# Kernel tuning notes

Hardware: AMD Instinct MI355X
Metric: run time of the kernel (lower is better)

The kernel has to match this reference:

```python
import jax, jax.numpy as jnp
import numpy as np

D_MODEL = 512
SEQ_LEN = 2048
S = 32  # local window size
BATCH = 2


def setup_inputs() -> dict:
    key = jax.random.key(0)
    ks = jax.random.split(key, 12)
    shp = (SEQ_LEN, BATCH, D_MODEL)
    return {
        "query": jax.random.normal(ks[0], shp, jnp.float32),
        "key": jax.random.normal(ks[1], shp, jnp.float32),
        "value": jax.random.normal(ks[2], shp, jnp.float32),
        "Wq": jax.random.normal(ks[3], (D_MODEL, D_MODEL), jnp.float32) * 0.02,
        "bq": jax.random.normal(ks[4], (D_MODEL,), jnp.float32) * 0.01,
        "Wk": jax.random.normal(ks[5], (D_MODEL, D_MODEL), jnp.float32) * 0.02,
        "bk": jax.random.normal(ks[6], (D_MODEL,), jnp.float32) * 0.01,
        "Wv": jax.random.normal(ks[7], (D_MODEL, D_MODEL), jnp.float32) * 0.02,
        "bv": jax.random.normal(ks[8], (D_MODEL,), jnp.float32) * 0.01,
        "pos_bias": jax.random.normal(ks[9], (SEQ_LEN, SEQ_LEN), jnp.float32) * 0.02,
        "Wo": jax.random.normal(ks[10], (D_MODEL, D_MODEL), jnp.float32) * 0.02,
        "bo": jax.random.normal(ks[11], (D_MODEL,), jnp.float32) * 0.01,
    }


def _aft_local(query, key, value, Wq, bq, Wk, bk, Wv, bv, pos_bias, Wo, bo):
    T, B, D = query.shape
    q = query @ Wq.T + bq  # [T,B,D]
    k = key @ Wk.T + bk
    v = value @ Wv.T + bv
    pb = pos_bias[:T, :T]

    # max_logit: elementwise max of per-dim key max and (key + col-max of pos_bias) max,
    # then batch index 0 (faithful to original `[0]` indexing) -> shape [D]
    max_logit = jnp.maximum(k.max(axis=0),
                            (k + pb.max(axis=0)[:, None, None]).max(axis=0))[0]

    # out-of-window running sums: tokens t' <= t - S contribute exp(k) (no pos bias)
    ek = jnp.exp(k - max_logit)                 # [T,B,D]
    cs_num = jnp.cumsum(ek * v, axis=0)
    cs_den = jnp.cumsum(ek, axis=0)
    t_arr = jnp.arange(T)
    prefix_idx = jnp.clip(t_arr - S, 0, T - 1)
    has_prefix = (t_arr >= S)[:, None, None]
    num_out = jnp.where(has_prefix, cs_num[prefix_idx], 0.0)
    den_out = jnp.where(has_prefix, cs_den[prefix_idx], 0.0)

    # in-window part: t' in [max(0, t-S+1), t] with pos_bias[t, t']
    j = jnp.arange(S)
    idx_raw = t_arr[:, None] - S + 1 + j[None, :]   # [T,S]
    valid = (idx_raw >= 0).astype(k.dtype)
    idx = jnp.clip(idx_raw, 0, T - 1)
    k_win = k[idx]                                  # [T,S,B,D]
    v_win = v[idx]                                  # [T,S,B,D]
    pb_win = pb[t_arr[:, None], idx]                # [T,S]
    exp_l = jnp.exp(k_win + pb_win[:, :, None, None] - max_logit) * valid[:, :, None, None]
    num_in = (exp_l * v_win).sum(axis=1)            # [T,B,D]
    den_in = exp_l.sum(axis=1)

    y = jax.nn.sigmoid(q) * (num_out + num_in) / (den_out + den_in)
    return y @ Wo.T + bo


def reference(query, key, value, Wq, bq, Wk, bk, Wv, bv, pos_bias, Wo, bo):
    return _aft_local(query, key, value, Wq, bq, Wk, bk, Wv, bv, pos_bias, Wo, bo)
```

## Files before the change

kernel.cpp:

```cpp
#include <hip/hip_runtime.h>
#include <hip/hip_bf16.h>

#define TT 2048
#define BB 2
#define DD 512
#define BD (BB*DD)
#define SS 32
#define MR (TT*BB)
#define NE (TT*BB*DD)
#define CH 32

typedef __bf16 bf16x8 __attribute__((ext_vector_type(8)));
typedef float f32x4 __attribute__((ext_vector_type(4)));
typedef float f32x2 __attribute__((ext_vector_type(2)));

__device__ __forceinline__ void async_copy16(void* lds, const void* gptr) {
    __builtin_amdgcn_global_load_lds(
        (const __attribute__((address_space(1))) void*)gptr,
        (__attribute__((address_space(3))) void*)lds,
        16, 0, 0);
}

#define MFMA16(a,b,c) __builtin_amdgcn_mfma_f32_16x16x32_bf16((a),(b),(c),0,0,0)

__global__ __launch_bounds__(256) void cast_all(
    const float* __restrict__ s0, const float* __restrict__ s1, const float* __restrict__ s2,
    const float* __restrict__ w0, const float* __restrict__ w1,
    const float* __restrict__ w2, const float* __restrict__ w3,
    __hip_bfloat16* __restrict__ d0, __hip_bfloat16* __restrict__ d1, __hip_bfloat16* __restrict__ d2,
    __hip_bfloat16* __restrict__ e0, __hip_bfloat16* __restrict__ e1,
    __hip_bfloat16* __restrict__ e2, __hip_bfloat16* __restrict__ e3)
{
    int b = blockIdx.x;
    const float* s;
    __hip_bfloat16* d;
    size_t i;
    if (b < 6144) {
        int which = b >> 11;
        s = which == 0 ? s0 : (which == 1 ? s1 : s2);
        d = which == 0 ? d0 : (which == 1 ? d1 : d2);
        i = ((size_t)(b & 2047) * 256 + threadIdx.x) * 4;
    } else {
        int b2 = b - 6144;
        int which = b2 >> 8;
        s = which == 0 ? w0 : (which == 1 ? w1 : (which == 2 ? w2 : w3));
        d = which == 0 ? e0 : (which == 1 ? e1 : (which == 2 ? e2 : e3));
        i = ((size_t)(b2 & 255) * 256 + threadIdx.x) * 4;
    }
    float4 f = *(const float4*)(s + i);
    union { __hip_bfloat16 h[4]; ushort4 u; } cv;
    cv.h[0] = __float2bfloat16(f.x); cv.h[1] = __float2bfloat16(f.y);
    cv.h[2] = __float2bfloat16(f.z); cv.h[3] = __float2bfloat16(f.w);
    *(ushort4*)((unsigned short*)d + i) = cv.u;
}

__global__ __launch_bounds__(256) void gemm_qkv(
    const __hip_bfloat16* __restrict__ qb, const __hip_bfloat16* __restrict__ kb,
    const __hip_bfloat16* __restrict__ vb,
    const __hip_bfloat16* __restrict__ Wqb, const __hip_bfloat16* __restrict__ Wkb,
    const __hip_bfloat16* __restrict__ Wvb,
    const float* __restrict__ bq, const float* __restrict__ bk,
    const float* __restrict__ bv,
    float* __restrict__ qout, float* __restrict__ ekn,
    float* __restrict__ part)
{
    __shared__ char smem[49152];
    const int tid = threadIdx.x;
    const int lane = tid & 63;
    const int wv = tid >> 6;
    const int wave_m = wv >> 1, wave_n = wv & 1;
    const int m0 = blockIdx.y * 64, n0 = blockIdx.x * 64;
    const int kq = lane >> 4, rr = lane & 15;

    if (blockIdx.z == 0) {
        f32x4 acc[2][2] = {};
        const __hip_bfloat16* Arow = qb + (size_t)(m0 + lane) * DD + wv * 8;
        const __hip_bfloat16* Wrow = Wqb + (size_t)(n0 + lane) * DD + wv * 8;
        async_copy16(smem + 0*8192 +        wv*1024, Arow + 0);
        async_copy16(smem + 0*8192 + 4096 + wv*1024, Wrow + 0);
        async_copy16(smem + 1*8192 +        wv*1024, Arow + 32);
        async_copy16(smem + 1*8192 + 4096 + wv*1024, Wrow + 32);
        asm volatile("s_waitcnt vmcnt(2)" ::: "memory");
        __builtin_amdgcn_s_barrier();
        #pragma unroll
        for (int it = 0; it < 16; ++it) {
            if (it + 2 < 16) {
                char* nb = smem + ((it + 2) % 3) * 8192;
                async_copy16(nb +        wv*1024, Arow + (it+2)*32);
                async_copy16(nb + 4096 + wv*1024, Wrow + (it+2)*32);
            }
            const char* cb = smem + (it % 3) * 8192;
            bf16x8 a0 = *(const bf16x8*)(cb + kq*1024 + (wave_m*32 +  0 + rr)*16);
            bf16x8 a1 = *(const bf16x8*)(cb + kq*1024 + (wave_m*32 + 16 + rr)*16);
            bf16x8 w0 = *(const bf16x8*)(cb + 4096 + kq*1024 + (wave_n*32 +  0 + rr)*16);
            bf16x8 w1 = *(const bf16x8*)(cb + 4096 + kq*1024 + (wave_n*32 + 16 + rr)*16);
            acc[0][0] = MFMA16(a0, w0, acc[0][0]);
            acc[0][1] = MFMA16(a0, w1, acc[0][1]);
            acc[1][0] = MFMA16(a1, w0, acc[1][0]);
            acc[1][1] = MFMA16(a1, w1, acc[1][1]);
            if (it < 15) {
                if (it < 14) asm volatile("s_waitcnt vmcnt(2) lgkmcnt(0)" ::: "memory");
                else         asm volatile("s_waitcnt vmcnt(0) lgkmcnt(0)" ::: "memory");
                __builtin_amdgcn_s_barrier();
            }
        }
        #pragma unroll
        for (int ms = 0; ms < 2; ++ms)
            #pragma unroll
            for (int ns = 0; ns < 2; ++ns) {
                int n = n0 + wave_n*32 + ns*16 + rr;
                float bn = bq[n];
                #pragma unroll
                for (int r = 0; r < 4; ++r) {
                    int m = m0 + wave_m*32 + ms*16 + kq*4 + r;
                    qout[(size_t)m * DD + n] = acc[ms][ns][r] + bn;
                }
            }
    } else {
        f32x4 acck[2][2] = {}, accv[2][2] = {};
        const __hip_bfloat16* AKrow = kb + (size_t)(m0 + lane) * DD + wv * 8;
        const __hip_bfloat16* WKrow = Wkb + (size_t)(n0 + lane) * DD + wv * 8;
        const __hip_bfloat16* AVrow = vb + (size_t)(m0 + lane) * DD + wv * 8;
        const __hip_bfloat16* WVrow = Wvb + (size_t)(n0 + lane) * DD + wv * 8;
        #pragma unroll
        for (int pt = 0; pt < 2; ++pt) {
            char* nb = smem + pt * 16384;
            async_copy16(nb +         wv*1024, AKrow + pt*32);
            async_copy16(nb +  4096 + wv*1024, WKrow + pt*32);
            async_copy16(nb +  8192 + wv*1024, AVrow + pt*32);
            async_copy16(nb + 12288 + wv*1024, WVrow + pt*32);
        }
        asm volatile("s_waitcnt vmcnt(4)" ::: "memory");
        __builtin_amdgcn_s_barrier();
        #pragma unroll
        for (int it = 0; it < 16; ++it) {
            if (it + 2 < 16) {
                char* nb = smem + ((it + 2) % 3) * 16384;
                async_copy16(nb +         wv*1024, AKrow + (it+2)*32);
                async_copy16(nb +  4096 + wv*1024, WKrow + (it+2)*32);
                async_copy16(nb +  8192 + wv*1024, AVrow + (it+2)*32);
                async_copy16(nb + 12288 + wv*1024, WVrow + (it+2)*32);
            }
            const char* cb = smem + (it % 3) * 16384;
            bf16x8 ak0 = *(const bf16x8*)(cb +         kq*1024 + (wave_m*32 +  0 + rr)*16);
            bf16x8 ak1 = *(const bf16x8*)(cb +         kq*1024 + (wave_m*32 + 16 + rr)*16);
            bf16x8 bk0 = *(const bf16x8*)(cb +  4096 + kq*1024 + (wave_n*32 +  0 + rr)*16);
            bf16x8 bk1 = *(const bf16x8*)(cb +  4096 + kq*1024 + (wave_n*32 + 16 + rr)*16);
            bf16x8 av0 = *(const bf16x8*)(cb +  8192 + kq*1024 + (wave_m*32 +  0 + rr)*16);
            bf16x8 av1 = *(const bf16x8*)(cb +  8192 + kq*1024 + (wave_m*32 + 16 + rr)*16);
            bf16x8 bv0 = *(const bf16x8*)(cb + 12288 + kq*1024 + (wave_n*32 +  0 + rr)*16);
            bf16x8 bv1 = *(const bf16x8*)(cb + 12288 + kq*1024 + (wave_n*32 + 16 + rr)*16);
            acck[0][0] = MFMA16(ak0, bk0, acck[0][0]);
            acck[0][1] = MFMA16(ak0, bk1, acck[0][1]);
            acck[1][0] = MFMA16(ak1, bk0, acck[1][0]);
            acck[1][1] = MFMA16(ak1, bk1, acck[1][1]);
            accv[0][0] = MFMA16(av0, bv0, accv[0][0]);
            accv[0][1] = MFMA16(av0, bv1, accv[0][1]);
            accv[1][0] = MFMA16(av1, bv0, accv[1][0]);
            accv[1][1] = MFMA16(av1, bv1, accv[1][1]);
            if (it < 15) {
                if (it < 14) asm volatile("s_waitcnt vmcnt(4) lgkmcnt(0)" ::: "memory");
                else         asm volatile("s_waitcnt vmcnt(0) lgkmcnt(0)" ::: "memory");
                __builtin_amdgcn_s_barrier();
            }
        }
        float sd[2][2] = {{0.f,0.f},{0.f,0.f}};
        float sn[2][2] = {{0.f,0.f},{0.f,0.f}};
        #pragma unroll
        for (int ms = 0; ms < 2; ++ms)
            #pragma unroll
            for (int ns = 0; ns < 2; ++ns) {
                int n = n0 + wave_n*32 + ns*16 + rr;
                float bkn = bk[n], bvn = bv[n];
                #pragma unroll
                for (int r = 0; r < 4; ++r) {
                    int m = m0 + wave_m*32 + ms*16 + kq*4 + r;
                    float e  = expf(acck[ms][ns][r] + bkn);
                    float nv = e * (accv[ms][ns][r] + bvn);
                    float2 st; st.x = e; st.y = nv;
                    *(float2*)&ekn[((size_t)m * DD + n) * 2] = st;
                    sd[ns][r & 1] += e;
                    sn[ns][r & 1] += nv;
                }
            }
        #pragma unroll
        for (int ns = 0; ns < 2; ++ns)
            #pragma unroll
            for (int par = 0; par < 2; ++par) {
                sd[ns][par] += __shfl_xor(sd[ns][par], 16, 64);
                sd[ns][par] += __shfl_xor(sd[ns][par], 32, 64);
                sn[ns][par] += __shfl_xor(sn[ns][par], 16, 64);
                sn[ns][par] += __shfl_xor(sn[ns][par], 32, 64);
            }
        __syncthreads();
        float* red = (float*)smem;
        if (lane < 16) {
            #pragma unroll
            for (int ns = 0; ns < 2; ++ns) {
                int c2 = wave_n*32 + ns*16 + rr;
                red[(0*2 + wave_m)*64 + c2] = sd[ns][0];
                red[(1*2 + wave_m)*64 + c2] = sd[ns][1];
                red[(2*2 + wave_m)*64 + c2] = sn[ns][0];
                red[(3*2 + wave_m)*64 + c2] = sn[ns][1];
            }
        }
        __syncthreads();
        {
            int which = tid >> 6;
            int c2 = tid & 63;
            float s = red[(which*2 + 0)*64 + c2] + red[(which*2 + 1)*64 + c2];
            int b = which & 1;
            int sel = which >> 1;
            part[((size_t)blockIdx.y * BD + b*512 + n0 + c2) * 2 + sel] = s;
        }
    }
}

__global__ __launch_bounds__(256, 1) void scan_part(
    const float* __restrict__ part, float* __restrict__ pref)
{
    const int col = blockIdx.x * 256 + threadIdx.x;
    f32x2 run = {0.f, 0.f};
    #pragma unroll
    for (int p0 = 0; p0 < 64; p0 += 8) {
        f32x2 v[8];
        #pragma unroll
        for (int u = 0; u < 8; ++u)
            v[u] = *(const f32x2*)&part[((size_t)(p0 + u) * BD + col) * 2];
        #pragma unroll
        for (int u = 0; u < 8; ++u) {
            *(f32x2*)&pref[((size_t)(p0 + u) * BD + col) * 2] = run;
            run += v[u];
        }
    }
}

__global__ __launch_bounds__(256, 3) void fused_window(
    const float* __restrict__ q, const float* __restrict__ ekn,
    const float* __restrict__ pref, const float* __restrict__ pb,
    __hip_bfloat16* __restrict__ yb)
{
    __shared__ float Et[64 * 64 * 2];
    __shared__ float wl[CH][SS];
    const int tid = threadIdx.x;
    const int chunk = blockIdx.y;
    const int t0 = chunk * CH;
    const int col0 = blockIdx.x * 64;
    const int c = tid & 63;
    const int sg = tid >> 6;
    const int s0 = sg * 8;

    {
        const int ub = tid >> 5;
        const int cp = tid & 31;
        #pragma unroll
        for (int j = 0; j < 8; ++j) {
            int u = ub + j * 8;
            int t = t0 - 32 + u;
            if (t >= 0) {
                const void* g = (const void*)(ekn + ((size_t)t * BD + col0 + cp * 2) * 2);
                async_copy16((char*)Et + (tid >> 6) * 1024 + j * 4096, g);
            }
        }
        if (chunk == 0) {
            f32x4 z = {0.f, 0.f, 0.f, 0.f};
            #pragma unroll
            for (int j = 0; j < 4; ++j)
                *(f32x4*)((char*)Et + tid * 16 + j * 4096) = z;
        }
    }

    #pragma unroll
    for (int i = 0; i < (CH * SS) / 256; ++i) {
        int idx = tid + i * 256;
        int tl = idx >> 5, jj = idx & 31;
        int t = t0 + tl;
        int u2 = t - (SS - 1) + jj;
        float w = 0.f;
        if (u2 >= 0) w = expf(pb[(size_t)t * TT + u2]);
        wl[tl][jj] = w;
    }

    float qv[8];
    #pragma unroll
    for (int k = 0; k < 8; ++k)
        qv[k] = q[(size_t)(t0 + s0 + k) * BD + col0 + c];
    f32x2 P = *(const f32x2*)&pref[((size_t)chunk * BD + col0 + c) * 2];

    __syncthreads();

    f32x2 ring[39];
    #pragma unroll
    for (int i = 0; i < 39; ++i)
        ring[i] = *(const f32x2*)&Et[((s0 + 1 + i) * 64 + c) * 2];

    f32x2 cs = P;
    #pragma unroll
    for (int u = 0; u < 31; ++u)
        if (u >= s0) cs -= ring[u - s0];

    #pragma unroll
    for (int k = 0; k < 8; ++k) {
        int s = s0 + k;
        if (k > 0) cs += ring[k - 1];
        f32x2 acc = cs;
        #pragma unroll
        for (int j4 = 0; j4 < 8; ++j4) {
            float4 w4 = *(const float4*)&wl[s][j4 * 4];
            acc += w4.x * ring[k + j4*4 + 0];
            acc += w4.y * ring[k + j4*4 + 1];
            acc += w4.z * ring[k + j4*4 + 2];
            acc += w4.w * ring[k + j4*4 + 3];
        }
        float sig = 1.f / (1.f + expf(-qv[k]));
        yb[(size_t)(t0 + s) * BD + col0 + c] = __float2bfloat16(sig * acc.y / acc.x);
    }
}

__global__ __launch_bounds__(256) void gemm_out(
    const __hip_bfloat16* __restrict__ yb, const __hip_bfloat16* __restrict__ Wob,
    const float* __restrict__ bo, float* __restrict__ out)
{
    __shared__ char smem[24576];
    const int tid = threadIdx.x;
    const int lane = tid & 63;
    const int wv = tid >> 6;
    const int wave_m = wv >> 1, wave_n = wv & 1;
    const int m0 = blockIdx.y * 64, n0 = blockIdx.x * 64;
    const int kq = lane >> 4, rr = lane & 15;

    f32x4 acc[2][2] = {};
    const __hip_bfloat16* Arow = yb + (size_t)(m0 + lane) * DD + wv * 8;
    const __hip_bfloat16* Wrow = Wob + (size_t)(n0 + lane) * DD + wv * 8;

    async_copy16(smem + 0*8192 +        wv*1024, Arow + 0);
    async_copy16(smem + 0*8192 + 4096 + wv*1024, Wrow + 0);
    async_copy16(smem + 1*8192 +        wv*1024, Arow + 32);
    async_copy16(smem + 1*8192 + 4096 + wv*1024, Wrow + 32);
    asm volatile("s_waitcnt vmcnt(2)" ::: "memory");
    __builtin_amdgcn_s_barrier();
    #pragma unroll
    for (int it = 0; it < 16; ++it) {
        if (it + 2 < 16) {
            char* nb = smem + ((it + 2) % 3) * 8192;
            async_copy16(nb +        wv*1024, Arow + (it+2)*32);
            async_copy16(nb + 4096 + wv*1024, Wrow + (it+2)*32);
        }
        const char* cb = smem + (it % 3) * 8192;
        bf16x8 a0 = *(const bf16x8*)(cb + kq*1024 + (wave_m*32 +  0 + rr)*16);
        bf16x8 a1 = *(const bf16x8*)(cb + kq*1024 + (wave_m*32 + 16 + rr)*16);
        bf16x8 w0 = *(const bf16x8*)(cb + 4096 + kq*1024 + (wave_n*32 +  0 + rr)*16);
        bf16x8 w1 = *(const bf16x8*)(cb + 4096 + kq*1024 + (wave_n*32 + 16 + rr)*16);
        acc[0][0] = MFMA16(a0, w0, acc[0][0]);
        acc[0][1] = MFMA16(a0, w1, acc[0][1]);
        acc[1][0] = MFMA16(a1, w0, acc[1][0]);
        acc[1][1] = MFMA16(a1, w1, acc[1][1]);
        if (it < 15) {
            if (it < 14) asm volatile("s_waitcnt vmcnt(2) lgkmcnt(0)" ::: "memory");
            else         asm volatile("s_waitcnt vmcnt(0) lgkmcnt(0)" ::: "memory");
            __builtin_amdgcn_s_barrier();
        }
    }
    #pragma unroll
    for (int ms = 0; ms < 2; ++ms)
        #pragma unroll
        for (int ns = 0; ns < 2; ++ns) {
            int n = n0 + wave_n*32 + ns*16 + rr;
            float bn = bo[n];
            #pragma unroll
            for (int r = 0; r < 4; ++r) {
                int m = m0 + wave_m*32 + ms*16 + kq*4 + r;
                out[(size_t)m * DD + n] = acc[ms][ns][r] + bn;
            }
        }
}

extern "C" void kernel_launch(void* const* d_in, const int* in_sizes, int n_in,
                              void* d_out, int out_size, void* d_ws, size_t ws_size,
                              hipStream_t stream) {
    const float* query = (const float*)d_in[0];
    const float* key   = (const float*)d_in[1];
    const float* value = (const float*)d_in[2];
    const float* Wq    = (const float*)d_in[3];
    const float* bq    = (const float*)d_in[4];
    const float* Wk    = (const float*)d_in[5];
    const float* bk    = (const float*)d_in[6];
    const float* Wv    = (const float*)d_in[7];
    const float* bv    = (const float*)d_in[8];
    const float* pb    = (const float*)d_in[9];
    const float* Wo    = (const float*)d_in[10];
    const float* bo    = (const float*)d_in[11];
    float* out = (float*)d_out;

    float* ws = (float*)d_ws;
    float* q    = ws;
    float* ekn  = ws + (size_t)NE;
    float* part = ws + (size_t)3 * NE;
    float* pref = part + 131072;
    __hip_bfloat16* bfb = (__hip_bfloat16*)(pref + 131072);
    __hip_bfloat16* qb  = bfb;
    __hip_bfloat16* kb  = bfb + (size_t)NE;
    __hip_bfloat16* vb  = bfb + (size_t)2 * NE;
    __hip_bfloat16* yb  = bfb + (size_t)3 * NE;
    __hip_bfloat16* Wqb = bfb + (size_t)4 * NE;
    __hip_bfloat16* Wkb = Wqb + 262144;
    __hip_bfloat16* Wvb = Wkb + 262144;
    __hip_bfloat16* Wob = Wvb + 262144;

    cast_all<<<7168, 256, 0, stream>>>(query, key, value, Wq, Wk, Wv, Wo,
                                       qb, kb, vb, Wqb, Wkb, Wvb, Wob);

    gemm_qkv<<<dim3(DD / 64, MR / 64, 2), 256, 0, stream>>>(
        qb, kb, vb, Wqb, Wkb, Wvb, bq, bk, bv,
        q, ekn, part);

    scan_part<<<4, 256, 0, stream>>>(part, pref);

    fused_window<<<dim3(BD / 64, TT / CH), 256, 0, stream>>>(
        q, ekn, pref, pb, yb);

    gemm_out<<<dim3(DD / 64, MR / 64), 256, 0, stream>>>(yb, Wob, bo, out);
}
```

Baseline: 190.3 us.

## Fuse all stages into one persistent kernel with atomic grid barriers

Replaces the five separate launches (cast, QKV GEMM, prefix scan, window kernel, output GEMM) with one persistent kernel of 512 blocks that moves between phases through atomic-counter grid barriers. The separate scan kernel is dropped: each window tile now sums the earlier per-chunk partials itself through a small LDS reduction. Each block runs both the K/V and Q GEMM tiles for its output tile in turn, and handles two window tiles. The aim is to cut launch and inter-kernel gaps, at the cost of serialising work inside each block. It also depends on all 512 blocks being co-resident (2 per CU), otherwise the spin barriers deadlock.

```diff
diff --git a/kernel.cpp b/kernel.cpp
--- a/kernel.cpp
+++ b/kernel.cpp
@@ -23,59 +23,333 @@
 
 #define MFMA16(a,b,c) __builtin_amdgcn_mfma_f32_16x16x32_bf16((a),(b),(c),0,0,0)
 
-__global__ __launch_bounds__(256) void cast_all(
-    const float* __restrict__ s0, const float* __restrict__ s1, const float* __restrict__ s2,
-    const float* __restrict__ w0, const float* __restrict__ w1,
-    const float* __restrict__ w2, const float* __restrict__ w3,
-    __hip_bfloat16* __restrict__ d0, __hip_bfloat16* __restrict__ d1, __hip_bfloat16* __restrict__ d2,
-    __hip_bfloat16* __restrict__ e0, __hip_bfloat16* __restrict__ e1,
-    __hip_bfloat16* __restrict__ e2, __hip_bfloat16* __restrict__ e3)
-{
-    int b = blockIdx.x;
-    const float* s;
-    __hip_bfloat16* d;
-    size_t i;
-    if (b < 6144) {
-        int which = b >> 11;
-        s = which == 0 ? s0 : (which == 1 ? s1 : s2);
-        d = which == 0 ? d0 : (which == 1 ? d1 : d2);
-        i = ((size_t)(b & 2047) * 256 + threadIdx.x) * 4;
-    } else {
-        int b2 = b - 6144;
-        int which = b2 >> 8;
-        s = which == 0 ? w0 : (which == 1 ? w1 : (which == 2 ? w2 : w3));
-        d = which == 0 ? e0 : (which == 1 ? e1 : (which == 2 ? e2 : e3));
-        i = ((size_t)(b2 & 255) * 256 + threadIdx.x) * 4;
+__device__ __forceinline__ void grid_barrier(unsigned* ctr, unsigned target) {
+    __syncthreads();
+    if (threadIdx.x == 0) {
+        __hip_atomic_fetch_add(ctr, 1u, __ATOMIC_ACQ_REL, __HIP_MEMORY_SCOPE_AGENT);
+        while (__hip_atomic_load(ctr, __ATOMIC_ACQUIRE, __HIP_MEMORY_SCOPE_AGENT) < target) {
+            __builtin_amdgcn_s_sleep(2);
+        }
     }
-    float4 f = *(const float4*)(s + i);
-    union { __hip_bfloat16 h[4]; ushort4 u; } cv;
-    cv.h[0] = __float2bfloat16(f.x); cv.h[1] = __float2bfloat16(f.y);
-    cv.h[2] = __float2bfloat16(f.z); cv.h[3] = __float2bfloat16(f.w);
-    *(ushort4*)((unsigned short*)d + i) = cv.u;
+    __syncthreads();
+    __threadfence();
 }
 
-__global__ __launch_bounds__(256) void gemm_qkv(
-    const __hip_bfloat16* __restrict__ qb, const __hip_bfloat16* __restrict__ kb,
-    const __hip_bfloat16* __restrict__ vb,
-    const __hip_bfloat16* __restrict__ Wqb, const __hip_bfloat16* __restrict__ Wkb,
-    const __hip_bfloat16* __restrict__ Wvb,
-    const float* __restrict__ bq, const float* __restrict__ bk,
-    const float* __restrict__ bv,
-    float* __restrict__ qout, float* __restrict__ ekn,
-    float* __restrict__ part)
+__global__ __launch_bounds__(256, 2) void aft_mega(
+    const float* __restrict__ query, const float* __restrict__ key,
+    const float* __restrict__ value,
+    const float* __restrict__ Wq, const float* __restrict__ bq,
+    const float* __restrict__ Wk, const float* __restrict__ bk,
+    const float* __restrict__ Wv, const float* __restrict__ bv,
+    const float* __restrict__ pb,
+    const float* __restrict__ Wo, const float* __restrict__ bo,
+    float* __restrict__ out,
+    float* __restrict__ qf, float* __restrict__ ekn, float* __restrict__ part,
+    __hip_bfloat16* __restrict__ qb, __hip_bfloat16* __restrict__ kb,
+    __hip_bfloat16* __restrict__ vb, __hip_bfloat16* __restrict__ yb,
+    __hip_bfloat16* __restrict__ Wqb, __hip_bfloat16* __restrict__ Wkb,
+    __hip_bfloat16* __restrict__ Wvb, __hip_bfloat16* __restrict__ Wob,
+    unsigned* bar)
 {
     __shared__ char smem[49152];
     const int tid = threadIdx.x;
+    const int bid = blockIdx.x;
     const int lane = tid & 63;
     const int wv = tid >> 6;
-    const int wave_m = wv >> 1, wave_n = wv & 1;
-    const int m0 = blockIdx.y * 64, n0 = blockIdx.x * 64;
-    const int kq = lane >> 4, rr = lane & 15;
-
-    if (blockIdx.z == 0) {
+
+    {
+        #pragma unroll
+        for (int h = 0; h < 2; ++h) {
+            float4 f[7];
+            unsigned short* da[7];
+            #pragma unroll
+            for (int p = 0; p < 7; ++p) {
+                int u = (h * 7 + p) * 131072 + bid * 256 + tid;
+                const float* s; __hip_bfloat16* d; size_t i;
+                if (u < 1572864) {
+                    int which = u >> 19;
+                    s = which == 0 ? query : (which == 1 ? key : value);
+                    d = which == 0 ? qb : (which == 1 ? kb : vb);
+                    i = (size_t)(u & 524287) * 4;
+                } else {
+                    int u2 = u - 1572864;
+                    int which = u2 >> 16;
+                    s = which == 0 ? Wq : (which == 1 ? Wk : (which == 2 ? Wv : Wo));
+                    d = which == 0 ? Wqb : (which == 1 ? Wkb : (which == 2 ? Wvb : Wob));
+                    i = (size_t)(u2 & 65535) * 4;
+                }
+                f[p] = *(const float4*)(s + i);
+                da[p] = (unsigned short*)d + i;
+            }
+            #pragma unroll
+            for (int p = 0; p < 7; ++p) {
+                union { __hip_bfloat16 hh[4]; ushort4 u4; } cv;
+                cv.hh[0] = __float2bfloat16(f[p].x); cv.hh[1] = __float2bfloat16(f[p].y);
+                cv.hh[2] = __float2bfloat16(f[p].z); cv.hh[3] = __float2bfloat16(f[p].w);
+                *(ushort4*)da[p] = cv.u4;
+            }
+        }
+    }
+    grid_barrier(&bar[0], 512);
+
+    {
+        const int wave_m = wv >> 1, wave_n = wv & 1;
+        const int kq = lane >> 4, rr = lane & 15;
+        const int n0 = (bid & 7) * 64, m0 = (bid >> 3) * 64;
+
+        {
+            f32x4 acck[2][2] = {}, accv[2][2] = {};
+            const __hip_bfloat16* AKrow = kb + (size_t)(m0 + lane) * DD + wv * 8;
+            const __hip_bfloat16* WKrow = Wkb + (size_t)(n0 + lane) * DD + wv * 8;
+            const __hip_bfloat16* AVrow = vb + (size_t)(m0 + lane) * DD + wv * 8;
+            const __hip_bfloat16* WVrow = Wvb + (size_t)(n0 + lane) * DD + wv * 8;
+            #pragma unroll
+            for (int pt = 0; pt < 2; ++pt) {
+                char* nb = smem + pt * 16384;
+                async_copy16(nb +         wv*1024, AKrow + pt*32);
+                async_copy16(nb +  4096 + wv*1024, WKrow + pt*32);
+                async_copy16(nb +  8192 + wv*1024, AVrow + pt*32);
+                async_copy16(nb + 12288 + wv*1024, WVrow + pt*32);
+            }
+            asm volatile("s_waitcnt vmcnt(4)" ::: "memory");
+            __builtin_amdgcn_s_barrier();
+            #pragma unroll
+            for (int it = 0; it < 16; ++it) {
+                if (it + 2 < 16) {
+                    char* nb = smem + ((it + 2) % 3) * 16384;
+                    async_copy16(nb +         wv*1024, AKrow + (it+2)*32);
+                    async_copy16(nb +  4096 + wv*1024, WKrow + (it+2)*32);
+                    async_copy16(nb +  8192 + wv*1024, AVrow + (it+2)*32);
+                    async_copy16(nb + 12288 + wv*1024, WVrow + (it+2)*32);
+                }
+                const char* cb = smem + (it % 3) * 16384;
+                bf16x8 ak0 = *(const bf16x8*)(cb +         kq*1024 + (wave_m*32 +  0 + rr)*16);
+                bf16x8 ak1 = *(const bf16x8*)(cb +         kq*1024 + (wave_m*32 + 16 + rr)*16);
+                bf16x8 bk0 = *(const bf16x8*)(cb +  4096 + kq*1024 + (wave_n*32 +  0 + rr)*16);
+                bf16x8 bk1 = *(const bf16x8*)(cb +  4096 + kq*1024 + (wave_n*32 + 16 + rr)*16);
+                bf16x8 av0 = *(const bf16x8*)(cb +  8192 + kq*1024 + (wave_m*32 +  0 + rr)*16);
+                bf16x8 av1 = *(const bf16x8*)(cb +  8192 + kq*1024 + (wave_m*32 + 16 + rr)*16);
+                bf16x8 bv0 = *(const bf16x8*)(cb + 12288 + kq*1024 + (wave_n*32 +  0 + rr)*16);
+                bf16x8 bv1 = *(const bf16x8*)(cb + 12288 + kq*1024 + (wave_n*32 + 16 + rr)*16);
+                acck[0][0] = MFMA16(ak0, bk0, acck[0][0]);
+                acck[0][1] = MFMA16(ak0, bk1, acck[0][1]);
+                acck[1][0] = MFMA16(ak1, bk0, acck[1][0]);
+                acck[1][1] = MFMA16(ak1, bk1, acck[1][1]);
+                accv[0][0] = MFMA16(av0, bv0, accv[0][0]);
+                accv[0][1] = MFMA16(av0, bv1, accv[0][1]);
+                accv[1][0] = MFMA16(av1, bv0, accv[1][0]);
+                accv[1][1] = MFMA16(av1, bv1, accv[1][1]);
+                if (it < 15) {
+                    if (it < 14) asm volatile("s_waitcnt vmcnt(4) lgkmcnt(0)" ::: "memory");
+                    else         asm volatile("s_waitcnt vmcnt(0) lgkmcnt(0)" ::: "memory");
+                    __builtin_amdgcn_s_barrier();
+                }
+            }
+            float sd[2][2] = {{0.f,0.f},{0.f,0.f}};
+            float sn[2][2] = {{0.f,0.f},{0.f,0.f}};
+            #pragma unroll
+            for (int ms = 0; ms < 2; ++ms)
+                #pragma unroll
+                for (int ns = 0; ns < 2; ++ns) {
+                    int n = n0 + wave_n*32 + ns*16 + rr;
+                    float bkn = bk[n], bvn = bv[n];
+                    #pragma unroll
+                    for (int r = 0; r < 4; ++r) {
+                        int m = m0 + wave_m*32 + ms*16 + kq*4 + r;
+                        float e  = expf(acck[ms][ns][r] + bkn);
+                        float nv = e * (accv[ms][ns][r] + bvn);
+                        float2 st; st.x = e; st.y = nv;
+                        *(float2*)&ekn[((size_t)m * DD + n) * 2] = st;
+                        sd[ns][r & 1] += e;
+                        sn[ns][r & 1] += nv;
+                    }
+                }
+            #pragma unroll
+            for (int ns = 0; ns < 2; ++ns)
+                #pragma unroll
+                for (int par = 0; par < 2; ++par) {
+                    sd[ns][par] += __shfl_xor(sd[ns][par], 16, 64);
+                    sd[ns][par] += __shfl_xor(sd[ns][par], 32, 64);
+                    sn[ns][par] += __shfl_xor(sn[ns][par], 16, 64);
+                    sn[ns][par] += __shfl_xor(sn[ns][par], 32, 64);
+                }
+            __syncthreads();
+            float* red = (float*)smem;
+            if (lane < 16) {
+                #pragma unroll
+                for (int ns = 0; ns < 2; ++ns) {
+                    int c2 = wave_n*32 + ns*16 + rr;
+                    red[(0*2 + wave_m)*64 + c2] = sd[ns][0];
+                    red[(1*2 + wave_m)*64 + c2] = sd[ns][1];
+                    red[(2*2 + wave_m)*64 + c2] = sn[ns][0];
+                    red[(3*2 + wave_m)*64 + c2] = sn[ns][1];
+                }
+            }
+            __syncthreads();
+            {
+                int which = tid >> 6;
+                int c2 = tid & 63;
+                float s = red[(which*2 + 0)*64 + c2] + red[(which*2 + 1)*64 + c2];
+                int b = which & 1;
+                int sel = which >> 1;
+                part[((size_t)(bid >> 3) * BD + b*512 + n0 + c2) * 2 + sel] = s;
+            }
+        }
+        __syncthreads();
+
+        {
+            f32x4 acc[2][2] = {};
+            const __hip_bfloat16* Arow = qb + (size_t)(m0 + lane) * DD + wv * 8;
+            const __hip_bfloat16* Wrow = Wqb + (size_t)(n0 + lane) * DD + wv * 8;
+            async_copy16(smem + 0*8192 +        wv*1024, Arow + 0);
+            async_copy16(smem + 0*8192 + 4096 + wv*1024, Wrow + 0);
+            async_copy16(smem + 1*8192 +        wv*1024, Arow + 32);
+            async_copy16(smem + 1*8192 + 4096 + wv*1024, Wrow + 32);
+            asm volatile("s_waitcnt vmcnt(2)" ::: "memory");
+            __builtin_amdgcn_s_barrier();
+            #pragma unroll
+            for (int it = 0; it < 16; ++it) {
+                if (it + 2 < 16) {
+                    char* nb = smem + ((it + 2) % 3) * 8192;
+                    async_copy16(nb +        wv*1024, Arow + (it+2)*32);
+                    async_copy16(nb + 4096 + wv*1024, Wrow + (it+2)*32);
+                }
+                const char* cb = smem + (it % 3) * 8192;
+                bf16x8 a0 = *(const bf16x8*)(cb + kq*1024 + (wave_m*32 +  0 + rr)*16);
+                bf16x8 a1 = *(const bf16x8*)(cb + kq*1024 + (wave_m*32 + 16 + rr)*16);
+                bf16x8 w0 = *(const bf16x8*)(cb + 4096 + kq*1024 + (wave_n*32 +  0 + rr)*16);
+                bf16x8 w1 = *(const bf16x8*)(cb + 4096 + kq*1024 + (wave_n*32 + 16 + rr)*16);
+                acc[0][0] = MFMA16(a0, w0, acc[0][0]);
+                acc[0][1] = MFMA16(a0, w1, acc[0][1]);
+                acc[1][0] = MFMA16(a1, w0, acc[1][0]);
+                acc[1][1] = MFMA16(a1, w1, acc[1][1]);
+                if (it < 15) {
+                    if (it < 14) asm volatile("s_waitcnt vmcnt(2) lgkmcnt(0)" ::: "memory");
+                    else         asm volatile("s_waitcnt vmcnt(0) lgkmcnt(0)" ::: "memory");
+                    __builtin_amdgcn_s_barrier();
+                }
+            }
+            #pragma unroll
+            for (int ms = 0; ms < 2; ++ms)
+                #pragma unroll
+                for (int ns = 0; ns < 2; ++ns) {
+                    int n = n0 + wave_n*32 + ns*16 + rr;
+                    float bn = bq[n];
+                    #pragma unroll
+                    for (int r = 0; r < 4; ++r) {
+                        int m = m0 + wave_m*32 + ms*16 + kq*4 + r;
+                        qf[(size_t)m * DD + n] = acc[ms][ns][r] + bn;
+                    }
+                }
+        }
+    }
+    grid_barrier(&bar[1], 512);
+
+    {
+        float* Et = (float*)smem;
+        float* wl = (float*)(smem + 32768);
+        float* red = (float*)(smem + 36864);
+        const int c = tid & 63;
+        const int sg = tid >> 6;
+        const int s0 = sg * 8;
+
+        #pragma unroll
+        for (int ti = 0; ti < 2; ++ti) {
+            const int tile = bid + ti * 512;
+            const int chunk = tile >> 4;
+            const int t0 = chunk * CH;
+            const int col0 = (tile & 15) * 64;
+            __syncthreads();
+
+            {
+                const int cp = tid & 31;
+                #pragma unroll
+                for (int j = 0; j < 8; ++j) {
+                    int u = (tid >> 5) + j * 8;
+                    int t = t0 - 32 + u;
+                    if (t >= 0) {
+                        const void* g = (const void*)(ekn + ((size_t)t * BD + col0 + cp * 2) * 2);
+                        async_copy16((char*)Et + wv * 1024 + j * 4096, g);
+                    }
+                }
+                if (chunk == 0) {
+                    f32x4 z = {0.f, 0.f, 0.f, 0.f};
+                    #pragma unroll
+                    for (int j = 0; j < 4; ++j)
+                        *(f32x4*)((char*)Et + tid * 16 + j * 4096) = z;
+                }
+            }
+
+            #pragma unroll
+            for (int i = 0; i < (CH * SS) / 256; ++i) {
+                int idx = tid + i * 256;
+                int tl = idx >> 5, jj = idx & 31;
+                int t = t0 + tl;
+                int u2 = t - (SS - 1) + jj;
+                float w = 0.f;
+                if (u2 >= 0) w = expf(pb[(size_t)t * TT + u2]);
+                wl[tl * SS + jj] = w;
+            }
+
+            float qv[8];
+            #pragma unroll
+            for (int k = 0; k < 8; ++k)
+                qv[k] = qf[(size_t)(t0 + s0 + k) * BD + col0 + c];
+            f32x2 acc2 = {0.f, 0.f};
+            #pragma unroll
+            for (int j = 0; j < 16; ++j) {
+                int p = sg + 4 * j;
+                if (p < chunk)
+                    acc2 += *(const f32x2*)&part[((size_t)p * BD + col0 + c) * 2];
+            }
+            *(f32x2*)&red[(sg * 64 + c) * 2] = acc2;
+
+            __syncthreads();
+
+            f32x2 P = *(const f32x2*)&red[(0 * 64 + c) * 2];
+            P += *(const f32x2*)&red[(1 * 64 + c) * 2];
+            P += *(const f32x2*)&red[(2 * 64 + c) * 2];
+            P += *(const f32x2*)&red[(3 * 64 + c) * 2];
+
+            f32x2 ring[39];
+            #pragma unroll
+            for (int i = 0; i < 39; ++i)
+                ring[i] = *(const f32x2*)&Et[((s0 + 1 + i) * 64 + c) * 2];
+
+            f32x2 cs = P;
+            #pragma unroll
+            for (int u = 0; u < 31; ++u)
+                if (u >= s0) cs -= ring[u - s0];
+
+            #pragma unroll
+            for (int k = 0; k < 8; ++k) {
+                int s = s0 + k;
+                if (k > 0) cs += ring[k - 1];
+                f32x2 acc = cs;
+                #pragma unroll
+                for (int j4 = 0; j4 < 8; ++j4) {
+                    float4 w4 = *(const float4*)&wl[s * SS + j4 * 4];
+                    acc += w4.x * ring[k + j4*4 + 0];
+                    acc += w4.y * ring[k + j4*4 + 1];
+                    acc += w4.z * ring[k + j4*4 + 2];
+                    acc += w4.w * ring[k + j4*4 + 3];
+                }
+                float sig = 1.f / (1.f + expf(-qv[k]));
+                yb[(size_t)(t0 + s) * BD + col0 + c] = __float2bfloat16(sig * acc.y / acc.x);
+            }
+        }
+    }
+    grid_barrier(&bar[2], 512);
+
+    {
+        const int wave_m = wv >> 1, wave_n = wv & 1;
+        const int kq = lane >> 4, rr = lane & 15;
+        const int n0 = (bid & 7) * 64, m0 = (bid >> 3) * 64;
+
         f32x4 acc[2][2] = {};
-        const __hip_bfloat16* Arow = qb + (size_t)(m0 + lane) * DD + wv * 8;
-        const __hip_bfloat16* Wrow = Wqb + (size_t)(n0 + lane) * DD + wv * 8;
+        const __hip_bfloat16* Arow = yb + (size_t)(m0 + lane) * DD + wv * 8;
+        const __hip_bfloat16* Wrow = Wob + (size_t)(n0 + lane) * DD + wv * 8;
+
         async_copy16(smem + 0*8192 +        wv*1024, Arow + 0);
         async_copy16(smem + 0*8192 + 4096 + wv*1024, Wrow + 0);
         async_copy16(smem + 1*8192 +        wv*1024, Arow + 32);
@@ -109,270 +383,14 @@
             #pragma unroll
             for (int ns = 0; ns < 2; ++ns) {
                 int n = n0 + wave_n*32 + ns*16 + rr;
-                float bn = bq[n];
+                float bn = bo[n];
                 #pragma unroll
                 for (int r = 0; r < 4; ++r) {
                     int m = m0 + wave_m*32 + ms*16 + kq*4 + r;
-                    qout[(size_t)m * DD + n] = acc[ms][ns][r] + bn;
-                }
-            }
-    } else {
-        f32x4 acck[2][2] = {}, accv[2][2] = {};
-        const __hip_bfloat16* AKrow = kb + (size_t)(m0 + lane) * DD + wv * 8;
-        const __hip_bfloat16* WKrow = Wkb + (size_t)(n0 + lane) * DD + wv * 8;
-        const __hip_bfloat16* AVrow = vb + (size_t)(m0 + lane) * DD + wv * 8;
-        const __hip_bfloat16* WVrow = Wvb + (size_t)(n0 + lane) * DD + wv * 8;
-        #pragma unroll
-        for (int pt = 0; pt < 2; ++pt) {
-            char* nb = smem + pt * 16384;
-            async_copy16(nb +         wv*1024, AKrow + pt*32);
-            async_copy16(nb +  4096 + wv*1024, WKrow + pt*32);
-            async_copy16(nb +  8192 + wv*1024, AVrow + pt*32);
-            async_copy16(nb + 12288 + wv*1024, WVrow + pt*32);
-        }
-        asm volatile("s_waitcnt vmcnt(4)" ::: "memory");
-        __builtin_amdgcn_s_barrier();
-        #pragma unroll
-        for (int it = 0; it < 16; ++it) {
-            if (it + 2 < 16) {
-                char* nb = smem + ((it + 2) % 3) * 16384;
-                async_copy16(nb +         wv*1024, AKrow + (it+2)*32);
-                async_copy16(nb +  4096 + wv*1024, WKrow + (it+2)*32);
-                async_copy16(nb +  8192 + wv*1024, AVrow + (it+2)*32);
-                async_copy16(nb + 12288 + wv*1024, WVrow + (it+2)*32);
-            }
-            const char* cb = smem + (it % 3) * 16384;
-            bf16x8 ak0 = *(const bf16x8*)(cb +         kq*1024 + (wave_m*32 +  0 + rr)*16);
-            bf16x8 ak1 = *(const bf16x8*)(cb +         kq*1024 + (wave_m*32 + 16 + rr)*16);
-            bf16x8 bk0 = *(const bf16x8*)(cb +  4096 + kq*1024 + (wave_n*32 +  0 + rr)*16);
-            bf16x8 bk1 = *(const bf16x8*)(cb +  4096 + kq*1024 + (wave_n*32 + 16 + rr)*16);
-            bf16x8 av0 = *(const bf16x8*)(cb +  8192 + kq*1024 + (wave_m*32 +  0 + rr)*16);
-            bf16x8 av1 = *(const bf16x8*)(cb +  8192 + kq*1024 + (wave_m*32 + 16 + rr)*16);
-            bf16x8 bv0 = *(const bf16x8*)(cb + 12288 + kq*1024 + (wave_n*32 +  0 + rr)*16);
-            bf16x8 bv1 = *(const bf16x8*)(cb + 12288 + kq*1024 + (wave_n*32 + 16 + rr)*16);
-            acck[0][0] = MFMA16(ak0, bk0, acck[0][0]);
-            acck[0][1] = MFMA16(ak0, bk1, acck[0][1]);
-            acck[1][0] = MFMA16(ak1, bk0, acck[1][0]);
-            acck[1][1] = MFMA16(ak1, bk1, acck[1][1]);
-            accv[0][0] = MFMA16(av0, bv0, accv[0][0]);
-            accv[0][1] = MFMA16(av0, bv1, accv[0][1]);
-            accv[1][0] = MFMA16(av1, bv0, accv[1][0]);
-            accv[1][1] = MFMA16(av1, bv1, accv[1][1]);
-            if (it < 15) {
-                if (it < 14) asm volatile("s_waitcnt vmcnt(4) lgkmcnt(0)" ::: "memory");
-                else         asm volatile("s_waitcnt vmcnt(0) lgkmcnt(0)" ::: "memory");
-                __builtin_amdgcn_s_barrier();
-            }
-        }
-        float sd[2][2] = {{0.f,0.f},{0.f,0.f}};
-        float sn[2][2] = {{0.f,0.f},{0.f,0.f}};
-        #pragma unroll
-        for (int ms = 0; ms < 2; ++ms)
-            #pragma unroll
-            for (int ns = 0; ns < 2; ++ns) {
-                int n = n0 + wave_n*32 + ns*16 + rr;
-                float bkn = bk[n], bvn = bv[n];
-                #pragma unroll
-                for (int r = 0; r < 4; ++r) {
-                    int m = m0 + wave_m*32 + ms*16 + kq*4 + r;
-                    float e  = expf(acck[ms][ns][r] + bkn);
-                    float nv = e * (accv[ms][ns][r] + bvn);
-                    float2 st; st.x = e; st.y = nv;
-                    *(float2*)&ekn[((size_t)m * DD + n) * 2] = st;
-                    sd[ns][r & 1] += e;
-                    sn[ns][r & 1] += nv;
-                }
-            }
-        #pragma unroll
-        for (int ns = 0; ns < 2; ++ns)
-            #pragma unroll
-            for (int par = 0; par < 2; ++par) {
-                sd[ns][par] += __shfl_xor(sd[ns][par], 16, 64);
-                sd[ns][par] += __shfl_xor(sd[ns][par], 32, 64);
-                sn[ns][par] += __shfl_xor(sn[ns][par], 16, 64);
-                sn[ns][par] += __shfl_xor(sn[ns][par], 32, 64);
-            }
-        __syncthreads();
-        float* red = (float*)smem;
-        if (lane < 16) {
-            #pragma unroll
-            for (int ns = 0; ns < 2; ++ns) {
-                int c2 = wave_n*32 + ns*16 + rr;
-                red[(0*2 + wave_m)*64 + c2] = sd[ns][0];
-                red[(1*2 + wave_m)*64 + c2] = sd[ns][1];
-                red[(2*2 + wave_m)*64 + c2] = sn[ns][0];
-                red[(3*2 + wave_m)*64 + c2] = sn[ns][1];
-            }
-        }
-        __syncthreads();
-        {
-            int which = tid >> 6;
-            int c2 = tid & 63;
-            float s = red[(which*2 + 0)*64 + c2] + red[(which*2 + 1)*64 + c2];
-            int b = which & 1;
-            int sel = which >> 1;
-            part[((size_t)blockIdx.y * BD + b*512 + n0 + c2) * 2 + sel] = s;
-        }
+                    out[(size_t)m * DD + n] = acc[ms][ns][r] + bn;
+                }
+            }
     }
-}
-
-__global__ __launch_bounds__(256, 1) void scan_part(
-    const float* __restrict__ part, float* __restrict__ pref)
-{
-    const int col = blockIdx.x * 256 + threadIdx.x;
-    f32x2 run = {0.f, 0.f};
-    #pragma unroll
-    for (int p0 = 0; p0 < 64; p0 += 8) {
-        f32x2 v[8];
-        #pragma unroll
-        for (int u = 0; u < 8; ++u)
-            v[u] = *(const f32x2*)&part[((size_t)(p0 + u) * BD + col) * 2];
-        #pragma unroll
-        for (int u = 0; u < 8; ++u) {
-            *(f32x2*)&pref[((size_t)(p0 + u) * BD + col) * 2] = run;
-            run += v[u];
-        }
-    }
-}
-
-__global__ __launch_bounds__(256, 3) void fused_window(
-    const float* __restrict__ q, const float* __restrict__ ekn,
-    const float* __restrict__ pref, const float* __restrict__ pb,
-    __hip_bfloat16* __restrict__ yb)
-{
-    __shared__ float Et[64 * 64 * 2];
-    __shared__ float wl[CH][SS];
-    const int tid = threadIdx.x;
-    const int chunk = blockIdx.y;
-    const int t0 = chunk * CH;
-    const int col0 = blockIdx.x * 64;
-    const int c = tid & 63;
-    const int sg = tid >> 6;
-    const int s0 = sg * 8;
-
-    {
-        const int ub = tid >> 5;
-        const int cp = tid & 31;
-        #pragma unroll
-        for (int j = 0; j < 8; ++j) {
-            int u = ub + j * 8;
-            int t = t0 - 32 + u;
-            if (t >= 0) {
-                const void* g = (const void*)(ekn + ((size_t)t * BD + col0 + cp * 2) * 2);
-                async_copy16((char*)Et + (tid >> 6) * 1024 + j * 4096, g);
-            }
-        }
-        if (chunk == 0) {
-            f32x4 z = {0.f, 0.f, 0.f, 0.f};
-            #pragma unroll
-            for (int j = 0; j < 4; ++j)
-                *(f32x4*)((char*)Et + tid * 16 + j * 4096) = z;
-        }
-    }
-
-    #pragma unroll
-    for (int i = 0; i < (CH * SS) / 256; ++i) {
-        int idx = tid + i * 256;
-        int tl = idx >> 5, jj = idx & 31;
-        int t = t0 + tl;
-        int u2 = t - (SS - 1) + jj;
-        float w = 0.f;
-        if (u2 >= 0) w = expf(pb[(size_t)t * TT + u2]);
-        wl[tl][jj] = w;
-    }
-
-    float qv[8];
-    #pragma unroll
-    for (int k = 0; k < 8; ++k)
-        qv[k] = q[(size_t)(t0 + s0 + k) * BD + col0 + c];
-    f32x2 P = *(const f32x2*)&pref[((size_t)chunk * BD + col0 + c) * 2];
-
-    __syncthreads();
-
-    f32x2 ring[39];
-    #pragma unroll
-    for (int i = 0; i < 39; ++i)
-        ring[i] = *(const f32x2*)&Et[((s0 + 1 + i) * 64 + c) * 2];
-
-    f32x2 cs = P;
-    #pragma unroll
-    for (int u = 0; u < 31; ++u)
-        if (u >= s0) cs -= ring[u - s0];
-
-    #pragma unroll
-    for (int k = 0; k < 8; ++k) {
-        int s = s0 + k;
-        if (k > 0) cs += ring[k - 1];
-        f32x2 acc = cs;
-        #pragma unroll
-        for (int j4 = 0; j4 < 8; ++j4) {
-            float4 w4 = *(const float4*)&wl[s][j4 * 4];
-            acc += w4.x * ring[k + j4*4 + 0];
-            acc += w4.y * ring[k + j4*4 + 1];
-            acc += w4.z * ring[k + j4*4 + 2];
-            acc += w4.w * ring[k + j4*4 + 3];
-        }
-        float sig = 1.f / (1.f + expf(-qv[k]));
-        yb[(size_t)(t0 + s) * BD + col0 + c] = __float2bfloat16(sig * acc.y / acc.x);
-    }
-}
-
-__global__ __launch_bounds__(256) void gemm_out(
-    const __hip_bfloat16* __restrict__ yb, const __hip_bfloat16* __restrict__ Wob,
-    const float* __restrict__ bo, float* __restrict__ out)
-{
-    __shared__ char smem[24576];
-    const int tid = threadIdx.x;
-    const int lane = tid & 63;
-    const int wv = tid >> 6;
-    const int wave_m = wv >> 1, wave_n = wv & 1;
-    const int m0 = blockIdx.y * 64, n0 = blockIdx.x * 64;
-    const int kq = lane >> 4, rr = lane & 15;
-
-    f32x4 acc[2][2] = {};
-    const __hip_bfloat16* Arow = yb + (size_t)(m0 + lane) * DD + wv * 8;
-    const __hip_bfloat16* Wrow = Wob + (size_t)(n0 + lane) * DD + wv * 8;
-
-    async_copy16(smem + 0*8192 +        wv*1024, Arow + 0);
-    async_copy16(smem + 0*8192 + 4096 + wv*1024, Wrow + 0);
-    async_copy16(smem + 1*8192 +        wv*1024, Arow + 32);
-    async_copy16(smem + 1*8192 + 4096 + wv*1024, Wrow + 32);
-    asm volatile("s_waitcnt vmcnt(2)" ::: "memory");
-    __builtin_amdgcn_s_barrier();
-    #pragma unroll
-    for (int it = 0; it < 16; ++it) {
-        if (it + 2 < 16) {
-            char* nb = smem + ((it + 2) % 3) * 8192;
-            async_copy16(nb +        wv*1024, Arow + (it+2)*32);
-            async_copy16(nb + 4096 + wv*1024, Wrow + (it+2)*32);
-        }
-        const char* cb = smem + (it % 3) * 8192;
-        bf16x8 a0 = *(const bf16x8*)(cb + kq*1024 + (wave_m*32 +  0 + rr)*16);
-        bf16x8 a1 = *(const bf16x8*)(cb + kq*1024 + (wave_m*32 + 16 + rr)*16);
-        bf16x8 w0 = *(const bf16x8*)(cb + 4096 + kq*1024 + (wave_n*32 +  0 + rr)*16);
-        bf16x8 w1 = *(const bf16x8*)(cb + 4096 + kq*1024 + (wave_n*32 + 16 + rr)*16);
-        acc[0][0] = MFMA16(a0, w0, acc[0][0]);
-        acc[0][1] = MFMA16(a0, w1, acc[0][1]);
-        acc[1][0] = MFMA16(a1, w0, acc[1][0]);
-        acc[1][1] = MFMA16(a1, w1, acc[1][1]);
-        if (it < 15) {
-            if (it < 14) asm volatile("s_waitcnt vmcnt(2) lgkmcnt(0)" ::: "memory");
-            else         asm volatile("s_waitcnt vmcnt(0) lgkmcnt(0)" ::: "memory");
-            __builtin_amdgcn_s_barrier();
-        }
-    }
-    #pragma unroll
-    for (int ms = 0; ms < 2; ++ms)
-        #pragma unroll
-        for (int ns = 0; ns < 2; ++ns) {
-            int n = n0 + wave_n*32 + ns*16 + rr;
-            float bn = bo[n];
-            #pragma unroll
-            for (int r = 0; r < 4; ++r) {
-                int m = m0 + wave_m*32 + ms*16 + kq*4 + r;
-                out[(size_t)m * DD + n] = acc[ms][ns][r] + bn;
-            }
-        }
 }
 
 extern "C" void kernel_launch(void* const* d_in, const int* in_sizes, int n_in,
@@ -393,11 +411,10 @@
     float* out = (float*)d_out;
 
     float* ws = (float*)d_ws;
-    float* q    = ws;
+    float* qf   = ws;
     float* ekn  = ws + (size_t)NE;
     float* part = ws + (size_t)3 * NE;
-    float* pref = part + 131072;
-    __hip_bfloat16* bfb = (__hip_bfloat16*)(pref + 131072);
+    __hip_bfloat16* bfb = (__hip_bfloat16*)(part + 131072);
     __hip_bfloat16* qb  = bfb;
     __hip_bfloat16* kb  = bfb + (size_t)NE;
     __hip_bfloat16* vb  = bfb + (size_t)2 * NE;
@@ -406,18 +423,12 @@
     __hip_bfloat16* Wkb = Wqb + 262144;
     __hip_bfloat16* Wvb = Wkb + 262144;
     __hip_bfloat16* Wob = Wvb + 262144;
-
-    cast_all<<<7168, 256, 0, stream>>>(query, key, value, Wq, Wk, Wv, Wo,
-                                       qb, kb, vb, Wqb, Wkb, Wvb, Wob);
-
-    gemm_qkv<<<dim3(DD / 64, MR / 64, 2), 256, 0, stream>>>(
-        qb, kb, vb, Wqb, Wkb, Wvb, bq, bk, bv,
-        q, ekn, part);
-
-    scan_part<<<4, 256, 0, stream>>>(part, pref);
-
-    fused_window<<<dim3(BD / 64, TT / CH), 256, 0, stream>>>(
-        q, ekn, pref, pb, yb);
-
-    gemm_out<<<dim3(DD / 64, MR / 64), 256, 0, stream>>>(yb, Wob, bo, out);
+    unsigned* bar = (unsigned*)(Wob + 262144);
+
+    hipMemsetAsync(bar, 0, 64, stream);
+
+    aft_mega<<<512, 256, 0, stream>>>(
+        query, key, value, Wq, bq, Wk, bk, Wv, bv, pb, Wo, bo,
+        out, qf, ekn, part,
+        qb, kb, vb, yb, Wqb, Wkb, Wvb, Wob, bar);
 }
```

New measurement: 472.7 us. 2.48x slower.
